# Optimization experiments

Hardware: AMD Instinct MI355X
Metric: run time of the kernel (lower is better)

## Reference

```python
import jax, jax.numpy as jnp
import numpy as np

B, S, F, D = 2, 576, 16, 512   # batch, spatial tokens (24x24), frames, query_dim
H, C = 8, 64                   # heads, dim_head; inner = H*C = 512


def setup_inputs() -> dict:
    key = jax.random.key(0)
    ks = jax.random.split(key, 6)
    x = jax.random.normal(ks[0], (B, S, F, D), jnp.float32)
    # alternating drop pattern over frames 2..F-1; identical per batch row,
    # as the module requires (it reshapes kept indices to [bs, -1] and takes
    # valid_num from row 0)
    pat = jnp.tile(jnp.array([1, 0], jnp.int64), (F - 2) // 2)
    drop_mask = jnp.broadcast_to(pat, (B, F - 2))
    sd = 1.0 / np.sqrt(D)
    Wq = jax.random.normal(ks[1], (D, H * C), jnp.float32) * sd
    Wk = jax.random.normal(ks[2], (D, H * C), jnp.float32) * sd
    Wv = jax.random.normal(ks[3], (D, H * C), jnp.float32) * sd
    Wout = jax.random.normal(ks[4], (H * C, D), jnp.float32) * (1.0 / np.sqrt(H * C))
    bout = jnp.zeros((D,), jnp.float32)
    return {"x": x, "drop_mask": drop_mask, "Wq": Wq, "Wk": Wk, "Wv": Wv,
            "Wout": Wout, "bout": bout}


def _sdpa(q, k, v):
    # q: [..., Lq, C], k/v: [..., Lk, C]; xformers default scale = 1/sqrt(C)
    scale = 1.0 / np.sqrt(q.shape[-1])
    logits = jnp.einsum('...qc,...kc->...qk', q, k) * scale
    w = jax.nn.softmax(logits, axis=-1)
    return jnp.einsum('...qk,...kc->...qc', w, v)


def reference(x, drop_mask, Wq, Wk, Wv, Wout, bout):
    b, s, f, _ = x.shape
    h, c = H, C
    q = x @ Wq  # [b, s, f, h*c]
    k = x @ Wk
    v = x @ Wv

    # ---- per-frame spatial self-attention for frames 1: ('b s f (h c) -> (b f h) s c')
    def to_bfhsc(t, nf):
        return t.reshape(b, s, nf, h, c).transpose(0, 2, 3, 1, 4)  # b f h s c

    ress = _sdpa(to_bfhsc(q[:, :, 1:], f - 1),
                 to_bfhsc(k[:, :, 1:], f - 1),
                 to_bfhsc(v[:, :, 1:], f - 1))            # [b, f-1, h, s, c]
    ress = ress.transpose(0, 3, 1, 2, 4).reshape(b, s, f - 1, h * c)

    # ---- frame-0 temporal attention over first 2 frames + non-dropped frames
    dm = np.asarray(drop_mask)
    valid = int((f - 2) - dm[0].sum())
    # kept frame indices (into frames 2..f-1), per batch row
    kept = np.stack([np.nonzero(dm[i] == 0)[0] for i in range(b)])  # [b, valid]
    idx = jnp.asarray(kept)[:, None, :, None]
    ka, va = k[:, :, 2:], v[:, :, 2:]                     # [b, s, f-2, h*c]
    ki = jnp.take_along_axis(ka, jnp.broadcast_to(idx, (b, s, valid, h * c)), axis=2)
    vi = jnp.take_along_axis(va, jnp.broadcast_to(idx, (b, s, valid, h * c)), axis=2)
    dk = jnp.concatenate([k[:, :, :2], ki], axis=2)        # [b, s, df, h*c]
    dv = jnp.concatenate([v[:, :, :2], vi], axis=2)
    df = 2 + valid

    qt = q[:, :, 0].reshape(b, s, h, c).transpose(0, 2, 1, 3)  # [b, h, s, c]
    kt = dk.reshape(b, s, df, h, c).transpose(0, 3, 1, 2, 4).reshape(b, h, s * df, c)
    vt = dv.reshape(b, s, df, h, c).transpose(0, 3, 1, 2, 4).reshape(b, h, s * df, c)
    resq = _sdpa(qt, kt, vt)                               # [b, h, s, c]
    resq = resq.transpose(0, 2, 1, 3).reshape(b, s, 1, h * c)

    res = jnp.concatenate([resq, ress], axis=2)            # [b, s, f, h*c]
    return res @ Wout + bout                               # [b, s, f, D]
```

## Files before the change

### kernel.cpp

```cpp
#include <hip/hip_runtime.h>
#include <math.h>

#define Bb 2
#define Ss 576
#define Ff 16
#define Hh 8
#define Cc 64
#define HC 512
#define Mrows (Bb * Ss * Ff)

typedef __bf16 bf16x8 __attribute__((ext_vector_type(8)));
typedef float  f32x4  __attribute__((ext_vector_type(4)));
typedef unsigned short u16;
typedef unsigned int   u32;

#if __has_builtin(__builtin_amdgcn_exp2f)
#define EXP2(x) __builtin_amdgcn_exp2f(x)
#else
#define EXP2(x) exp2f(x)
#endif

#define QSCALE 0.18033688011112042f

__device__ __forceinline__ u16 f2bf(float f) {
    union { __bf16 b; u16 u; } cv;
    cv.b = (__bf16)f;
    return cv.u;
}

__device__ __forceinline__ int swz8(int row, int g) {
    return row * 64 + (((g ^ (row & 7) ^ (((row >> 3) & 1) << 1)) & 7) << 3);
}
__device__ __forceinline__ int swzg(int row, int g) {
    return row * 32 + (((g ^ (row & 3)) & 3) << 3);
}

__global__ __launch_bounds__(256) void convert_x_kernel(
    const float* __restrict__ x, u16* __restrict__ xb)
{
    size_t idx = ((size_t)blockIdx.x * 256 + threadIdx.x) * 8;
    f32x4 a = *(const f32x4*)&x[idx];
    f32x4 b = *(const f32x4*)&x[idx + 4];
    union { u16 s[8]; uint4 v; } u;
#pragma unroll
    for (int j = 0; j < 4; ++j) u.s[j] = f2bf(a[j]);
#pragma unroll
    for (int j = 0; j < 4; ++j) u.s[4 + j] = f2bf(b[j]);
    *(uint4*)&xb[idx] = u.v;
}

__global__ __launch_bounds__(256) void convert_w_kernel(
    const float* __restrict__ W0, const float* __restrict__ W1,
    const float* __restrict__ W2, const float* __restrict__ W3,
    u16* __restrict__ Wt)
{
    __shared__ float Ts[64][65];
    const int mz = blockIdx.z;
    const float* W = (mz == 0) ? W0 : (mz == 1) ? W1 : (mz == 2) ? W2 : W3;
    u16* Wo = Wt + (size_t)mz * 512 * 512;
    const int k0 = blockIdx.x * 64, n0 = blockIdx.y * 64;
    const int t = threadIdx.x;
#pragma unroll
    for (int p = 0; p < 4; ++p) {
        int idx = t + p * 256;
        int row = idx >> 4, cg = idx & 15;
        *(float4*)&Ts[row][cg * 4] =
            *(const float4*)&W[(size_t)(k0 + row) * 512 + n0 + cg * 4];
    }
    __syncthreads();
#pragma unroll
    for (int p = 0; p < 2; ++p) {
        int idx = t + p * 256;
        int row = idx >> 3, cg = idx & 7;
        union { u16 s[8]; uint4 v; } u;
#pragma unroll
        for (int j = 0; j < 8; ++j) u.s[j] = f2bf(Ts[cg * 8 + j][row]);
        *(uint4*)&Wo[(size_t)(n0 + row) * 512 + k0 + cg * 8] = u.v;
    }
}

template <int OUT_BF16>
__device__ __forceinline__ void gemm_body(
    const u16* __restrict__ A, const u16* __restrict__ Wt,
    const float* __restrict__ bias, float scale, void* __restrict__ Cout,
    int mt, int nt)
{
    __shared__ u16 As[128 * 32];
    __shared__ u16 Bs[128 * 32];
    const int t = threadIdx.x;
    const int w = t >> 6, L = t & 63;
    const int m0 = mt * 128, n0 = nt * 128;
    const int wm = (w >> 1) * 64, wn = (w & 1) * 64;

    const int srow = t >> 2, scg = t & 3;
    const u16* Ap = A  + (size_t)(m0 + srow) * 512 + scg * 8;
    const u16* Bp = Wt + (size_t)(n0 + srow) * 512 + scg * 8;
    const int lo0 = swzg(srow, scg), lo1 = swzg(srow + 64, scg);

    uint4 ua0 = *(const uint4*)(Ap);
    uint4 ua1 = *(const uint4*)(Ap + 64 * 512);
    uint4 ub0 = *(const uint4*)(Bp);
    uint4 ub1 = *(const uint4*)(Bp + 64 * 512);

    f32x4 acc[4][4];
#pragma unroll
    for (int i = 0; i < 4; ++i)
#pragma unroll
        for (int j = 0; j < 4; ++j) acc[i][j] = (f32x4){0.f, 0.f, 0.f, 0.f};

    for (int k0 = 0; k0 < 512; k0 += 32) {
        __syncthreads();
        *(uint4*)&As[lo0] = ua0;
        *(uint4*)&As[lo1] = ua1;
        *(uint4*)&Bs[lo0] = ub0;
        *(uint4*)&Bs[lo1] = ub1;
        __syncthreads();
        if (k0 < 480) {
            const u16* ap = Ap + k0 + 32;
            const u16* bp = Bp + k0 + 32;
            ua0 = *(const uint4*)(ap);
            ua1 = *(const uint4*)(ap + 64 * 512);
            ub0 = *(const uint4*)(bp);
            ub1 = *(const uint4*)(bp + 64 * 512);
        }
        bf16x8 af[4], bfr[4];
#pragma unroll
        for (int i = 0; i < 4; ++i) {
            af[i]  = *(const bf16x8*)&As[swzg(wm + 16 * i + (L & 15), L >> 4)];
            bfr[i] = *(const bf16x8*)&Bs[swzg(wn + 16 * i + (L & 15), L >> 4)];
        }
#pragma unroll
        for (int i = 0; i < 4; ++i)
#pragma unroll
            for (int j = 0; j < 4; ++j)
                acc[i][j] = __builtin_amdgcn_mfma_f32_16x16x32_bf16(
                    af[i], bfr[j], acc[i][j], 0, 0, 0);
    }

#pragma unroll
    for (int i = 0; i < 4; ++i)
#pragma unroll
        for (int j = 0; j < 4; ++j)
#pragma unroll
            for (int r = 0; r < 4; ++r) {
                int row = m0 + wm + 16 * i + (L >> 4) * 4 + r;
                int col = n0 + wn + 16 * j + (L & 15);
                float vv = acc[i][j][r] * scale;
                if (OUT_BF16) {
                    float pvv = __shfl_xor(vv, 1);
                    if (!(L & 1)) {
                        u32 pk2 = (u32)f2bf(vv) | ((u32)f2bf(pvv) << 16);
                        *(u32*)((u16*)Cout + (size_t)row * 512 + col) = pk2;
                    }
                } else {
                    ((float*)Cout)[(size_t)row * 512 + col] = vv + bias[col];
                }
            }
}

__global__ __launch_bounds__(256) void gemm_qkv_kernel(
    const u16* __restrict__ xb, const u16* __restrict__ Wt,
    u16* __restrict__ q, u16* __restrict__ k, u16* __restrict__ v)
{
    const int which = blockIdx.z;
    const u16* W = Wt + (size_t)which * 512 * 512;
    u16* C = (which == 0) ? q : (which == 1) ? k : v;
    float scale = (which == 0) ? QSCALE : 1.0f;
    gemm_body<1>(xb, W, nullptr, scale, C, blockIdx.x, blockIdx.y);
}

__global__ __launch_bounds__(256) void gemm_out_kernel(
    const u16* __restrict__ res, const u16* __restrict__ Wt3,
    const float* __restrict__ bout, float* __restrict__ out)
{
    gemm_body<0>(res, Wt3, bout, 1.0f, out, blockIdx.x, blockIdx.y);
}

__global__ __launch_bounds__(256) void transpose_v_kernel(
    const u16* __restrict__ v, u16* __restrict__ vT)
{
    __shared__ u16 Ts[64 * 72];
    int bid = blockIdx.x;
    const int st = bid % 9; bid /= 9;
    const int h = bid % Hh; bid /= Hh;
    const int f = bid % Ff;
    const int b = bid / Ff;
    const int t = threadIdx.x;
#pragma unroll
    for (int p = 0; p < 2; ++p) {
        int idx = t + p * 256;
        int row = idx >> 3, cg = idx & 7;
        *(uint4*)&Ts[row * 72 + cg * 8] =
            *(const uint4*)&v[(size_t)((b * Ss + st * 64 + row) * Ff + f) * HC + h * Cc + cg * 8];
    }
    __syncthreads();
#pragma unroll
    for (int p = 0; p < 2; ++p) {
        int idx = t + p * 256;
        int c = idx >> 3, sg = idx & 7;
        union { u16 s[8]; uint4 u4; } u;
#pragma unroll
        for (int j = 0; j < 8; ++j) u.s[j] = Ts[(sg * 8 + j) * 72 + c];
        *(uint4*)&vT[((size_t)((b * Ff + f) * Hh + h) * Cc + c) * Ss + st * 64 + sg * 8] = u.u4;
    }
}

__global__ __launch_bounds__(256) void attn_kernel(
    const u16* __restrict__ q, const u16* __restrict__ k,
    const u16* __restrict__ vT, const int* __restrict__ dm,
    u16* __restrict__ res)
{
    __shared__ u16 Qs[64 * 64];
    __shared__ u16 Ks[64 * 64];
    __shared__ u16 Vts[64 * 64];
    __shared__ u16 Ps[64 * 64];
    __shared__ int fl[16];
    __shared__ int df_s;

    const int t = threadIdx.x;
    const int w = t >> 6, L = t & 63;
    const int bi = blockIdx.x;

    int b, h, qt, qframe, mode;
    if (bi < Bb * Hh * 9) {
        mode = 0;
        b = bi / (Hh * 9);
        int r = bi % (Hh * 9);
        h = r / 9; qt = r % 9; qframe = 0;
    } else {
        mode = 1;
        int idx = bi - Bb * Hh * 9;
        b = idx / ((Ff - 1) * Hh * 9);
        int r = idx % ((Ff - 1) * Hh * 9);
        int fi = r / (Hh * 9);
        int r2 = r % (Hh * 9);
        h = r2 / 9; qt = r2 % 9; qframe = 1 + fi;
    }

    if (t == 0) {
        if (mode == 0) {
            int n = 0;
            fl[n++] = 0; fl[n++] = 1;
            for (int j = 0; j < Ff - 2; ++j)
                if (dm[b * (Ff - 2) + j] == 0) fl[n++] = 2 + j;
            df_s = n;
        } else df_s = 1;
    }

    const int srow = t >> 3, scg = t & 7;

#pragma unroll
    for (int p = 0; p < 2; ++p) {
        int row = srow + p * 32;
        *(uint4*)&Qs[swz8(row, scg)] =
            *(const uint4*)&q[(size_t)((b * Ss + qt * 64 + row) * Ff + qframe) * HC + h * Cc + scg * 8];
    }
    __syncthreads();

    const int nkt = (mode == 0) ? df_s * 9 : 9;

    bf16x8 aq0 = *(const bf16x8*)&Qs[swz8(16 * w + (L & 15), (L >> 4))];
    bf16x8 aq1 = *(const bf16x8*)&Qs[swz8(16 * w + (L & 15), (L >> 4) + 4)];

    float lsum[4] = {0.f, 0.f, 0.f, 0.f};
    f32x4 o[4];
#pragma unroll
    for (int c = 0; c < 4; ++c) o[c] = (f32x4){0.f, 0.f, 0.f, 0.f};

    uint4 pk0, pk1, pv0, pv1;
    {
        int kf = (mode == 0) ? fl[0] : qframe;
        const u16* kpp = k + (size_t)((b * Ss + srow) * Ff + kf) * HC + h * Cc + scg * 8;
        pk0 = *(const uint4*)kpp;
        pk1 = *(const uint4*)(kpp + (size_t)32 * Ff * HC);
        const u16* vpp = vT + ((size_t)((b * Ff + kf) * Hh + h) * Cc + srow) * Ss + scg * 8;
        pv0 = *(const uint4*)vpp;
        pv1 = *(const uint4*)(vpp + (size_t)32 * Ss);
    }

    const int lko0 = swz8(srow, scg), lko1 = swz8(srow + 32, scg);

    for (int kt = 0; kt < nkt; ++kt) {
        __syncthreads();
        *(uint4*)&Ks[lko0]  = pk0;
        *(uint4*)&Ks[lko1]  = pk1;
        *(uint4*)&Vts[lko0] = pv0;
        *(uint4*)&Vts[lko1] = pv1;
        __syncthreads();

        if (kt + 1 < nkt) {
            int kn = kt + 1, kf, s0;
            if (mode == 0) { int fi = kn / 9; kf = fl[fi]; s0 = (kn - fi * 9) * 64; }
            else           { kf = qframe;     s0 = kn * 64; }
            const u16* kpp = k + (size_t)((b * Ss + s0 + srow) * Ff + kf) * HC + h * Cc + scg * 8;
            pk0 = *(const uint4*)kpp;
            pk1 = *(const uint4*)(kpp + (size_t)32 * Ff * HC);
            const u16* vpp = vT + ((size_t)((b * Ff + kf) * Hh + h) * Cc + srow) * Ss + s0 + scg * 8;
            pv0 = *(const uint4*)vpp;
            pv1 = *(const uint4*)(vpp + (size_t)32 * Ss);
        }

        f32x4 s[4];
#pragma unroll
        for (int n = 0; n < 4; ++n) s[n] = (f32x4){0.f, 0.f, 0.f, 0.f};
#pragma unroll
        for (int n = 0; n < 4; ++n) {
            bf16x8 bk0 = *(const bf16x8*)&Ks[swz8(n * 16 + (L & 15), (L >> 4))];
            bf16x8 bk1 = *(const bf16x8*)&Ks[swz8(n * 16 + (L & 15), (L >> 4) + 4)];
            s[n] = __builtin_amdgcn_mfma_f32_16x16x32_bf16(aq0, bk0, s[n], 0, 0, 0);
            s[n] = __builtin_amdgcn_mfma_f32_16x16x32_bf16(aq1, bk1, s[n], 0, 0, 0);
        }

#pragma unroll
        for (int n = 0; n < 4; ++n) {
            int colg = n * 2 + ((L & 15) >> 3);
#pragma unroll
            for (int r = 0; r < 4; ++r) {
                float p = EXP2(s[n][r]);
                lsum[r] += p;
                int row = 16 * w + (L >> 4) * 4 + r;
                Ps[row * 64 +
                   (((colg ^ (row & 7) ^ (((row >> 3) & 1) << 1)) & 7) << 3) +
                   (L & 7)] = f2bf(p);
            }
        }

        bf16x8 pa0 = *(const bf16x8*)&Ps[swz8(16 * w + (L & 15), (L >> 4))];
        bf16x8 pa1 = *(const bf16x8*)&Ps[swz8(16 * w + (L & 15), (L >> 4) + 4)];
#pragma unroll
        for (int c = 0; c < 4; ++c) {
            bf16x8 bv0 = *(const bf16x8*)&Vts[swz8(c * 16 + (L & 15), (L >> 4))];
            bf16x8 bv1 = *(const bf16x8*)&Vts[swz8(c * 16 + (L & 15), (L >> 4) + 4)];
            o[c] = __builtin_amdgcn_mfma_f32_16x16x32_bf16(pa0, bv0, o[c], 0, 0, 0);
            o[c] = __builtin_amdgcn_mfma_f32_16x16x32_bf16(pa1, bv1, o[c], 0, 0, 0);
        }
    }

#pragma unroll
    for (int d = 1; d < 16; d <<= 1)
#pragma unroll
        for (int r = 0; r < 4; ++r) lsum[r] += __shfl_xor(lsum[r], d);
    float inv[4];
#pragma unroll
    for (int r = 0; r < 4; ++r) inv[r] = 1.f / lsum[r];

#pragma unroll
    for (int c = 0; c < 4; ++c)
#pragma unroll
        for (int r = 0; r < 4; ++r) {
            float val = o[c][r] * inv[r];
            float pvv = __shfl_xor(val, 1);
            if (!(L & 1)) {
                int sq = qt * 64 + 16 * w + (L >> 4) * 4 + r;
                int col = h * Cc + c * 16 + (L & 15);
                u32 pk2 = (u32)f2bf(val) | ((u32)f2bf(pvv) << 16);
                *(u32*)&res[(size_t)((b * Ss + sq) * Ff + qframe) * HC + col] = pk2;
            }
        }
}

extern "C" void kernel_launch(void* const* d_in, const int* in_sizes, int n_in,
                              void* d_out, int out_size, void* d_ws, size_t ws_size,
                              hipStream_t stream)
{
    (void)in_sizes; (void)n_in; (void)out_size; (void)ws_size;
    const float* x    = (const float*)d_in[0];
    const int*   dmsk = (const int*)  d_in[1];
    const float* Wq   = (const float*)d_in[2];
    const float* Wk   = (const float*)d_in[3];
    const float* Wv   = (const float*)d_in[4];
    const float* Wout = (const float*)d_in[5];
    const float* bout = (const float*)d_in[6];
    float* out = (float*)d_out;

    const size_t NE = (size_t)Mrows * HC;
    u16* xb  = (u16*)d_ws;
    u16* q   = xb  + NE;
    u16* kk  = q   + NE;
    u16* vv  = kk  + NE;
    u16* vT  = vv  + NE;
    u16* res = vT  + NE;
    u16* Wt  = res + NE;

    convert_x_kernel<<<4608, 256, 0, stream>>>(x, xb);
    convert_w_kernel<<<dim3(8, 8, 4), 256, 0, stream>>>(Wq, Wk, Wv, Wout, Wt);
    gemm_qkv_kernel<<<dim3(144, 4, 3), 256, 0, stream>>>(xb, Wt, q, kk, vv);
    transpose_v_kernel<<<2304, 256, 0, stream>>>(vv, vT);
    attn_kernel<<<2304, 256, 0, stream>>>(q, kk, vT, dmsk, res);
    gemm_out_kernel<<<dim3(144, 4), 256, 0, stream>>>(
        res, Wt + (size_t)3 * 512 * 512, bout, out);
}
```

Baseline: 268.3 us.

## Fuse x conversion and V transpose into QKV GEMM, use frame-major layouts

The QKV GEMM now reads fp32 x directly and packs it to bf16 while staging tiles, so the separate x-conversion kernel goes away. The V projection writes its output already transposed into the vT layout, which removes the transpose kernel and the intermediate v buffer. q, k and res are stored frame-major (b,f,s,hc), and the attention kernel loads Q fragments straight from global memory instead of through shared memory. Block ordering is also changed to group heads and batches together. The cost is twice as many bytes of A-operand traffic per GEMM tile, since x is read as fp32, plus scattered 8-byte vT stores and index arithmetic in the epilogues.

```diff
diff --git a/kernel.cpp b/kernel.cpp
--- a/kernel.cpp
+++ b/kernel.cpp
@@ -35,18 +35,11 @@
     return row * 32 + (((g ^ (row & 3)) & 3) << 3);
 }
 
-__global__ __launch_bounds__(256) void convert_x_kernel(
-    const float* __restrict__ x, u16* __restrict__ xb)
-{
-    size_t idx = ((size_t)blockIdx.x * 256 + threadIdx.x) * 8;
-    f32x4 a = *(const f32x4*)&x[idx];
-    f32x4 b = *(const f32x4*)&x[idx + 4];
+__device__ __forceinline__ uint4 pack8(float4 a, float4 b) {
     union { u16 s[8]; uint4 v; } u;
-#pragma unroll
-    for (int j = 0; j < 4; ++j) u.s[j] = f2bf(a[j]);
-#pragma unroll
-    for (int j = 0; j < 4; ++j) u.s[4 + j] = f2bf(b[j]);
-    *(uint4*)&xb[idx] = u.v;
+    u.s[0] = f2bf(a.x); u.s[1] = f2bf(a.y); u.s[2] = f2bf(a.z); u.s[3] = f2bf(a.w);
+    u.s[4] = f2bf(b.x); u.s[5] = f2bf(b.y); u.s[6] = f2bf(b.z); u.s[7] = f2bf(b.w);
+    return u.v;
 }
 
 __global__ __launch_bounds__(256) void convert_w_kernel(
@@ -79,27 +72,128 @@
     }
 }
 
-template <int OUT_BF16>
-__device__ __forceinline__ void gemm_body(
-    const u16* __restrict__ A, const u16* __restrict__ Wt,
-    const float* __restrict__ bias, float scale, void* __restrict__ Cout,
-    int mt, int nt)
+__global__ __launch_bounds__(256) void qkv_kernel(
+    const float* __restrict__ x, const u16* __restrict__ Wt,
+    u16* __restrict__ q, u16* __restrict__ k, u16* __restrict__ vT)
 {
     __shared__ u16 As[128 * 32];
     __shared__ u16 Bs[128 * 32];
+    const int bi = blockIdx.x;
+    const int mt = bi % 144;
+    const int mm = bi / 144;
+    const int nt = mm & 3, mat = mm >> 2;
     const int t = threadIdx.x;
     const int w = t >> 6, L = t & 63;
     const int m0 = mt * 128, n0 = nt * 128;
     const int wm = (w >> 1) * 64, wn = (w & 1) * 64;
 
     const int srow = t >> 2, scg = t & 3;
-    const u16* Ap = A  + (size_t)(m0 + srow) * 512 + scg * 8;
-    const u16* Bp = Wt + (size_t)(n0 + srow) * 512 + scg * 8;
+    const int ma0 = m0 + srow, ma1 = m0 + srow + 64;
+    const int b0 = ma0 / 9216, r0 = ma0 % 9216, f0 = r0 / 576, s0 = r0 % 576;
+    const int b1 = ma1 / 9216, r1 = ma1 % 9216, f1 = r1 / 576, s1 = r1 % 576;
+    const float* xp0 = x + ((size_t)(b0 * 576 + s0) * 16 + f0) * 512 + scg * 8;
+    const float* xp1 = x + ((size_t)(b1 * 576 + s1) * 16 + f1) * 512 + scg * 8;
+    const u16* Bp = Wt + (size_t)mat * 512 * 512 + (size_t)(n0 + srow) * 512 + scg * 8;
     const int lo0 = swzg(srow, scg), lo1 = swzg(srow + 64, scg);
 
-    uint4 ua0 = *(const uint4*)(Ap);
+    float4 fa0 = *(const float4*)xp0, fa0b = *(const float4*)(xp0 + 4);
+    float4 fa1 = *(const float4*)xp1, fa1b = *(const float4*)(xp1 + 4);
+    uint4 ub0 = *(const uint4*)Bp;
+    uint4 ub1 = *(const uint4*)(Bp + 64 * 512);
+
+    f32x4 acc[4][4];
+#pragma unroll
+    for (int i = 0; i < 4; ++i)
+#pragma unroll
+        for (int j = 0; j < 4; ++j) acc[i][j] = (f32x4){0.f, 0.f, 0.f, 0.f};
+
+    for (int k0 = 0; k0 < 512; k0 += 32) {
+        __syncthreads();
+        *(uint4*)&As[lo0] = pack8(fa0, fa0b);
+        *(uint4*)&As[lo1] = pack8(fa1, fa1b);
+        *(uint4*)&Bs[lo0] = ub0;
+        *(uint4*)&Bs[lo1] = ub1;
+        __syncthreads();
+        if (k0 < 480) {
+            fa0  = *(const float4*)(xp0 + k0 + 32);
+            fa0b = *(const float4*)(xp0 + k0 + 36);
+            fa1  = *(const float4*)(xp1 + k0 + 32);
+            fa1b = *(const float4*)(xp1 + k0 + 36);
+            ub0  = *(const uint4*)(Bp + k0 + 32);
+            ub1  = *(const uint4*)(Bp + k0 + 32 + 64 * 512);
+        }
+        bf16x8 af[4], bfr[4];
+#pragma unroll
+        for (int i = 0; i < 4; ++i) {
+            af[i]  = *(const bf16x8*)&As[swzg(wm + 16 * i + (L & 15), L >> 4)];
+            bfr[i] = *(const bf16x8*)&Bs[swzg(wn + 16 * i + (L & 15), L >> 4)];
+        }
+#pragma unroll
+        for (int i = 0; i < 4; ++i)
+#pragma unroll
+            for (int j = 0; j < 4; ++j)
+                acc[i][j] = __builtin_amdgcn_mfma_f32_16x16x32_bf16(
+                    af[i], bfr[j], acc[i][j], 0, 0, 0);
+    }
+
+    if (mat < 2) {
+        u16* Cout = (mat == 0) ? q : k;
+        const float scale = (mat == 0) ? QSCALE : 1.0f;
+#pragma unroll
+        for (int i = 0; i < 4; ++i)
+#pragma unroll
+            for (int j = 0; j < 4; ++j)
+#pragma unroll
+                for (int r = 0; r < 4; ++r) {
+                    int row = m0 + wm + 16 * i + (L >> 4) * 4 + r;
+                    int col = n0 + wn + 16 * j + (L & 15);
+                    float vv = acc[i][j][r] * scale;
+                    float pvv = __shfl_xor(vv, 1);
+                    if (!(L & 1)) {
+                        u32 pk2 = (u32)f2bf(vv) | ((u32)f2bf(pvv) << 16);
+                        *(u32*)(Cout + (size_t)row * 512 + col) = pk2;
+                    }
+                }
+    } else {
+#pragma unroll
+        for (int i = 0; i < 4; ++i) {
+            int row = m0 + wm + 16 * i + (L >> 4) * 4;
+            int bb = row / 9216, rr = row % 9216;
+            int f = rr / 576, s = rr % 576;
+#pragma unroll
+            for (int j = 0; j < 4; ++j) {
+                int col = n0 + wn + 16 * j + (L & 15);
+                int h = col >> 6, c = col & 63;
+                union { u16 s4[4]; uint2 v; } u;
+#pragma unroll
+                for (int r = 0; r < 4; ++r) u.s4[r] = f2bf(acc[i][j][r]);
+                *(uint2*)&vT[((((size_t)(bb * 16 + f) * 8 + h) * 64 + c) * 576) + s] = u.v;
+            }
+        }
+    }
+}
+
+__global__ __launch_bounds__(256) void gemm_out_kernel(
+    const u16* __restrict__ res, const u16* __restrict__ Wt3,
+    const float* __restrict__ bout, float* __restrict__ out)
+{
+    __shared__ u16 As[128 * 32];
+    __shared__ u16 Bs[128 * 32];
+    const int bi = blockIdx.x;
+    const int mt = bi % 144, nt = bi / 144;
+    const int t = threadIdx.x;
+    const int w = t >> 6, L = t & 63;
+    const int m0 = mt * 128, n0 = nt * 128;
+    const int wm = (w >> 1) * 64, wn = (w & 1) * 64;
+
+    const int srow = t >> 2, scg = t & 3;
+    const u16* Ap = res + (size_t)(m0 + srow) * 512 + scg * 8;
+    const u16* Bp = Wt3 + (size_t)(n0 + srow) * 512 + scg * 8;
+    const int lo0 = swzg(srow, scg), lo1 = swzg(srow + 64, scg);
+
+    uint4 ua0 = *(const uint4*)Ap;
     uint4 ua1 = *(const uint4*)(Ap + 64 * 512);
-    uint4 ub0 = *(const uint4*)(Bp);
+    uint4 ub0 = *(const uint4*)Bp;
     uint4 ub1 = *(const uint4*)(Bp + 64 * 512);
 
     f32x4 acc[4][4];
@@ -116,12 +210,10 @@
         *(uint4*)&Bs[lo1] = ub1;
         __syncthreads();
         if (k0 < 480) {
-            const u16* ap = Ap + k0 + 32;
-            const u16* bp = Bp + k0 + 32;
-            ua0 = *(const uint4*)(ap);
-            ua1 = *(const uint4*)(ap + 64 * 512);
-            ub0 = *(const uint4*)(bp);
-            ub1 = *(const uint4*)(bp + 64 * 512);
+            ua0 = *(const uint4*)(Ap + k0 + 32);
+            ua1 = *(const uint4*)(Ap + k0 + 32 + 64 * 512);
+            ub0 = *(const uint4*)(Bp + k0 + 32);
+            ub1 = *(const uint4*)(Bp + k0 + 32 + 64 * 512);
         }
         bf16x8 af[4], bfr[4];
 #pragma unroll
@@ -140,69 +232,17 @@
 #pragma unroll
     for (int i = 0; i < 4; ++i)
 #pragma unroll
-        for (int j = 0; j < 4; ++j)
-#pragma unroll
-            for (int r = 0; r < 4; ++r) {
-                int row = m0 + wm + 16 * i + (L >> 4) * 4 + r;
+        for (int r = 0; r < 4; ++r) {
+            int row = m0 + wm + 16 * i + (L >> 4) * 4 + r;
+            int bb = row / 9216, rr = row % 9216;
+            int f = rr / 576, s = rr % 576;
+            size_t obase = ((size_t)(bb * 576 + s) * 16 + f) * 512;
+#pragma unroll
+            for (int j = 0; j < 4; ++j) {
                 int col = n0 + wn + 16 * j + (L & 15);
-                float vv = acc[i][j][r] * scale;
-                if (OUT_BF16) {
-                    float pvv = __shfl_xor(vv, 1);
-                    if (!(L & 1)) {
-                        u32 pk2 = (u32)f2bf(vv) | ((u32)f2bf(pvv) << 16);
-                        *(u32*)((u16*)Cout + (size_t)row * 512 + col) = pk2;
-                    }
-                } else {
-                    ((float*)Cout)[(size_t)row * 512 + col] = vv + bias[col];
-                }
+                out[obase + col] = acc[i][j][r] + bout[col];
             }
-}
-
-__global__ __launch_bounds__(256) void gemm_qkv_kernel(
-    const u16* __restrict__ xb, const u16* __restrict__ Wt,
-    u16* __restrict__ q, u16* __restrict__ k, u16* __restrict__ v)
-{
-    const int which = blockIdx.z;
-    const u16* W = Wt + (size_t)which * 512 * 512;
-    u16* C = (which == 0) ? q : (which == 1) ? k : v;
-    float scale = (which == 0) ? QSCALE : 1.0f;
-    gemm_body<1>(xb, W, nullptr, scale, C, blockIdx.x, blockIdx.y);
-}
-
-__global__ __launch_bounds__(256) void gemm_out_kernel(
-    const u16* __restrict__ res, const u16* __restrict__ Wt3,
-    const float* __restrict__ bout, float* __restrict__ out)
-{
-    gemm_body<0>(res, Wt3, bout, 1.0f, out, blockIdx.x, blockIdx.y);
-}
-
-__global__ __launch_bounds__(256) void transpose_v_kernel(
-    const u16* __restrict__ v, u16* __restrict__ vT)
-{
-    __shared__ u16 Ts[64 * 72];
-    int bid = blockIdx.x;
-    const int st = bid % 9; bid /= 9;
-    const int h = bid % Hh; bid /= Hh;
-    const int f = bid % Ff;
-    const int b = bid / Ff;
-    const int t = threadIdx.x;
-#pragma unroll
-    for (int p = 0; p < 2; ++p) {
-        int idx = t + p * 256;
-        int row = idx >> 3, cg = idx & 7;
-        *(uint4*)&Ts[row * 72 + cg * 8] =
-            *(const uint4*)&v[(size_t)((b * Ss + st * 64 + row) * Ff + f) * HC + h * Cc + cg * 8];
-    }
-    __syncthreads();
-#pragma unroll
-    for (int p = 0; p < 2; ++p) {
-        int idx = t + p * 256;
-        int c = idx >> 3, sg = idx & 7;
-        union { u16 s[8]; uint4 u4; } u;
-#pragma unroll
-        for (int j = 0; j < 8; ++j) u.s[j] = Ts[(sg * 8 + j) * 72 + c];
-        *(uint4*)&vT[((size_t)((b * Ff + f) * Hh + h) * Cc + c) * Ss + st * 64 + sg * 8] = u.u4;
-    }
+        }
 }
 
 __global__ __launch_bounds__(256) void attn_kernel(
@@ -210,7 +250,6 @@
     const u16* __restrict__ vT, const int* __restrict__ dm,
     u16* __restrict__ res)
 {
-    __shared__ u16 Qs[64 * 64];
     __shared__ u16 Ks[64 * 64];
     __shared__ u16 Vts[64 * 64];
     __shared__ u16 Ps[64 * 64];
@@ -222,19 +261,19 @@
     const int bi = blockIdx.x;
 
     int b, h, qt, qframe, mode;
-    if (bi < Bb * Hh * 9) {
+    if (bi < 144) {
         mode = 0;
-        b = bi / (Hh * 9);
-        int r = bi % (Hh * 9);
-        h = r / 9; qt = r % 9; qframe = 0;
+        qt = bi >> 4;
+        int g = bi & 15;
+        b = g >> 3; h = g & 7; qframe = 0;
     } else {
         mode = 1;
-        int idx = bi - Bb * Hh * 9;
-        b = idx / ((Ff - 1) * Hh * 9);
-        int r = idx % ((Ff - 1) * Hh * 9);
-        int fi = r / (Hh * 9);
-        int r2 = r % (Hh * 9);
-        h = r2 / 9; qt = r2 % 9; qframe = 1 + fi;
+        int u = bi - 144;
+        int g = u % 240;
+        qt = u / 240;
+        b = g / 120;
+        int rr = g % 120;
+        qframe = 1 + (rr >> 3); h = rr & 7;
     }
 
     if (t == 0) {
@@ -246,36 +285,30 @@
             df_s = n;
         } else df_s = 1;
     }
-
-    const int srow = t >> 3, scg = t & 7;
-
-#pragma unroll
-    for (int p = 0; p < 2; ++p) {
-        int row = srow + p * 32;
-        *(uint4*)&Qs[swz8(row, scg)] =
-            *(const uint4*)&q[(size_t)((b * Ss + qt * 64 + row) * Ff + qframe) * HC + h * Cc + scg * 8];
-    }
     __syncthreads();
 
     const int nkt = (mode == 0) ? df_s * 9 : 9;
 
-    bf16x8 aq0 = *(const bf16x8*)&Qs[swz8(16 * w + (L & 15), (L >> 4))];
-    bf16x8 aq1 = *(const bf16x8*)&Qs[swz8(16 * w + (L & 15), (L >> 4) + 4)];
+    const u16* qbase = q + ((size_t)(b * 16 + qframe) * 576 + qt * 64 + 16 * w + (L & 15)) * 512
+                         + h * 64 + (L >> 4) * 8;
+    bf16x8 aq0 = *(const bf16x8*)qbase;
+    bf16x8 aq1 = *(const bf16x8*)(qbase + 32);
 
     float lsum[4] = {0.f, 0.f, 0.f, 0.f};
     f32x4 o[4];
 #pragma unroll
     for (int c = 0; c < 4; ++c) o[c] = (f32x4){0.f, 0.f, 0.f, 0.f};
 
+    const int srow = t >> 3, scg = t & 7;
     uint4 pk0, pk1, pv0, pv1;
     {
-        int kf = (mode == 0) ? fl[0] : qframe;
-        const u16* kpp = k + (size_t)((b * Ss + srow) * Ff + kf) * HC + h * Cc + scg * 8;
+        int kf0 = (mode == 0) ? 0 : qframe;
+        const u16* kpp = k + ((size_t)(b * 16 + kf0) * 576 + srow) * 512 + h * 64 + scg * 8;
         pk0 = *(const uint4*)kpp;
-        pk1 = *(const uint4*)(kpp + (size_t)32 * Ff * HC);
-        const u16* vpp = vT + ((size_t)((b * Ff + kf) * Hh + h) * Cc + srow) * Ss + scg * 8;
+        pk1 = *(const uint4*)(kpp + 32 * 512);
+        const u16* vpp = vT + (((size_t)(b * 16 + kf0) * 8 + h) * 64 + srow) * 576 + scg * 8;
         pv0 = *(const uint4*)vpp;
-        pv1 = *(const uint4*)(vpp + (size_t)32 * Ss);
+        pv1 = *(const uint4*)(vpp + 32 * 576);
     }
 
     const int lko0 = swz8(srow, scg), lko1 = swz8(srow + 32, scg);
@@ -292,12 +325,12 @@
             int kn = kt + 1, kf, s0;
             if (mode == 0) { int fi = kn / 9; kf = fl[fi]; s0 = (kn - fi * 9) * 64; }
             else           { kf = qframe;     s0 = kn * 64; }
-            const u16* kpp = k + (size_t)((b * Ss + s0 + srow) * Ff + kf) * HC + h * Cc + scg * 8;
+            const u16* kpp = k + ((size_t)(b * 16 + kf) * 576 + s0 + srow) * 512 + h * 64 + scg * 8;
             pk0 = *(const uint4*)kpp;
-            pk1 = *(const uint4*)(kpp + (size_t)32 * Ff * HC);
-            const u16* vpp = vT + ((size_t)((b * Ff + kf) * Hh + h) * Cc + srow) * Ss + s0 + scg * 8;
+            pk1 = *(const uint4*)(kpp + 32 * 512);
+            const u16* vpp = vT + (((size_t)(b * 16 + kf) * 8 + h) * 64 + srow) * 576 + s0 + scg * 8;
             pv0 = *(const uint4*)vpp;
-            pv1 = *(const uint4*)(vpp + (size_t)32 * Ss);
+            pv1 = *(const uint4*)(vpp + 32 * 576);
         }
 
         f32x4 s[4];
@@ -353,8 +386,8 @@
             if (!(L & 1)) {
                 int sq = qt * 64 + 16 * w + (L >> 4) * 4 + r;
                 int col = h * Cc + c * 16 + (L & 15);
-                u32 pk2 = (u32)f2bf(val) | ((u32)f2bf(pvv) << 16);
-                *(u32*)&res[(size_t)((b * Ss + sq) * Ff + qframe) * HC + col] = pk2;
+                *(u32*)&res[((size_t)(b * 16 + qframe) * 576 + sq) * 512 + col] =
+                    (u32)f2bf(val) | ((u32)f2bf(pvv) << 16);
             }
         }
 }
@@ -374,19 +407,15 @@
     float* out = (float*)d_out;
 
     const size_t NE = (size_t)Mrows * HC;
-    u16* xb  = (u16*)d_ws;
-    u16* q   = xb  + NE;
+    u16* q   = (u16*)d_ws;
     u16* kk  = q   + NE;
-    u16* vv  = kk  + NE;
-    u16* vT  = vv  + NE;
+    u16* vT  = kk  + NE;
     u16* res = vT  + NE;
     u16* Wt  = res + NE;
 
-    convert_x_kernel<<<4608, 256, 0, stream>>>(x, xb);
     convert_w_kernel<<<dim3(8, 8, 4), 256, 0, stream>>>(Wq, Wk, Wv, Wout, Wt);
-    gemm_qkv_kernel<<<dim3(144, 4, 3), 256, 0, stream>>>(xb, Wt, q, kk, vv);
-    transpose_v_kernel<<<2304, 256, 0, stream>>>(vv, vT);
+    qkv_kernel<<<1728, 256, 0, stream>>>(x, Wt, q, kk, vT);
     attn_kernel<<<2304, 256, 0, stream>>>(q, kk, vT, dmsk, res);
-    gemm_out_kernel<<<dim3(144, 4), 256, 0, stream>>>(
+    gemm_out_kernel<<<576, 256, 0, stream>>>(
         res, Wt + (size_t)3 * 512 * 512, bout, out);
 }
```

Result: faster. 245.3 us (-8.6%).
